# Performance work log

Measured on AMD Instinct MI355X. Metric: run time of the kernel, lower is better.

Reference implementation:

```python
import jax, jax.numpy as jnp
import numpy as np

NUM_FILTER = 256
CAPS_LEN = 8
NUM_EMOTIONS = 8
OUT_DIM = 16
NUM_CHANNEL = 25
TIME_LEN = 25
NUM_CAPS = NUM_CHANNEL * TIME_LEN * (NUM_FILTER // CAPS_LEN)  # 20000
NUM_ITERATIONS = 3


def setup_inputs() -> dict:
    key = jax.random.key(0)
    ks = jax.random.split(key, 10)
    B = 32
    x = jax.random.normal(ks[0], (B, 54, 54), jnp.float32)
    conv1_w = jax.random.normal(ks[1], (NUM_FILTER, 1, 6, 6), jnp.float32) * 0.05
    conv1_b = jax.random.normal(ks[2], (NUM_FILTER,), jnp.float32) * 0.01
    conv2_w = jax.random.normal(ks[3], (NUM_FILTER, NUM_FILTER, 6, 6), jnp.float32) * 0.01
    conv2_b = jax.random.normal(ks[4], (NUM_FILTER,), jnp.float32) * 0.01
    conv3_w = jax.random.normal(ks[5], (NUM_FILTER, 2 * NUM_FILTER, 1, 1), jnp.float32) * 0.05
    conv3_b = jax.random.normal(ks[6], (NUM_FILTER,), jnp.float32) * 0.01
    # PrimaryCaps: one Linear(caps_len -> caps_len) per capsule, batched as [nc, out, in]
    pc_w = jax.random.normal(ks[7], (NUM_CAPS, CAPS_LEN, CAPS_LEN), jnp.float32) * 0.1
    pc_b = jax.random.normal(ks[8], (NUM_CAPS, CAPS_LEN), jnp.float32) * 0.1
    # EmotionCaps transform W: [nc, num_emotions, out_dim, in_dim]
    W = jax.random.normal(ks[9], (NUM_CAPS, NUM_EMOTIONS, OUT_DIM, CAPS_LEN), jnp.float32) * 0.05
    return {"x": x, "conv1_w": conv1_w, "conv1_b": conv1_b, "conv2_w": conv2_w,
            "conv2_b": conv2_b, "conv3_w": conv3_w, "conv3_b": conv3_b,
            "pc_w": pc_w, "pc_b": pc_b, "W": W}


def _conv(x, w, b, stride):
    y = jax.lax.conv_general_dilated(x, w, (stride, stride), 'VALID',
                                     dimension_numbers=('NCHW', 'OIHW', 'NCHW'))
    return y + b[None, :, None, None]


def _squash(s):
    # scale = |s|^2 / (1 + |s|^2); out = scale * s / (|s| + 1e-8)
    n2 = jnp.sum(s * s, axis=-1, keepdims=True)
    n = jnp.sqrt(n2)
    return (n2 / (1.0 + n2)) * s / (n + 1e-8)


def reference(x, conv1_w, conv1_b, conv2_w, conv2_b, conv3_w, conv3_b, pc_w, pc_b, W):
    x4 = x[:, None]                                    # [B,1,54,54]
    x1 = jax.nn.relu(_conv(x4, conv1_w, conv1_b, 2))   # [B,F,25,25]
    y = jnp.pad(x1, ((0, 0), (0, 0), (2, 3), (2, 3)))  # ZeroPad2d((2,3,2,3))
    y = jax.nn.relu(_conv(y, conv2_w, conv2_b, 1))     # [B,F,25,25]
    z = jax.nn.relu(jnp.concatenate([x1, y], axis=1))  # [B,2F,25,25]
    z = _conv(z, conv3_w, conv3_b, 1)                  # [B,F,25,25]
    B, F, H, Wd = z.shape
    # flatten to capsules: [B, F//caps_len, caps_len, H*W] -> [B, nc, caps_len]
    caps = z.reshape(B, F // CAPS_LEN, CAPS_LEN, H * Wd)
    caps = caps.transpose(0, 1, 3, 2).reshape(B, NUM_CAPS, CAPS_LEN)
    # PrimaryCaps: per-capsule linear, batched as a single einsum
    u = jnp.einsum('bni,noi->bno', caps, pc_w) + pc_b[None]   # [B,nc,caps_len]
    # EmotionCaps: u_hat[b,n,e,o] = W[n,e,o,i] u[b,n,i]
    u_hat = jnp.einsum('bni,neoi->bneo', u, W)                # [B,nc,ne,out_dim]
    b = jnp.zeros((B, NUM_CAPS, NUM_EMOTIONS), u.dtype)
    v = None
    for r in range(NUM_ITERATIONS):
        c = jax.nn.softmax(b, axis=2)[..., None]              # [B,nc,ne,1]
        v = _squash(jnp.sum(c * u_hat, axis=1))               # [B,ne,out_dim]
        if r < NUM_ITERATIONS - 1:
            b = b + jnp.einsum('bneo,beo->bne', u_hat, v)
    return jnp.linalg.norm(v, axis=-1)                        # [B,ne]
```

## Files before the change

kernel.cpp:

```cpp
#include <hip/hip_runtime.h>

typedef unsigned short u16;
typedef __attribute__((ext_vector_type(8))) short bf16x8;
typedef __attribute__((ext_vector_type(4))) float floatx4;

#define NPIX 625
#define NCAPS 20000
#define K2 9216

__device__ __forceinline__ u16 f2bf(float f) {
  unsigned u = __float_as_uint(f);
  return (u16)((u + 0x7fffu + ((u >> 16) & 1u)) >> 16);
}

__device__ __forceinline__ float bf2f(unsigned v) {
  return __uint_as_float(v << 16);
}

#define GLDS16(g, l) __builtin_amdgcn_global_load_lds( \
    (const __attribute__((address_space(1))) void*)(g), \
    (__attribute__((address_space(3))) void*)(l), 16, 0, 0)

__global__ void prep_weights2(const float* __restrict__ w2, const float* __restrict__ w3,
                              u16* __restrict__ A2, u16* __restrict__ A3) {
  if (blockIdx.x < 256) {
    const int oc = blockIdx.x, c = threadIdx.x;
    const float* src = w2 + (oc * 256 + c) * 36;
    float v[36];
#pragma unroll
    for (int k = 0; k < 9; k++) {
      const float4 q = *(const float4*)(src + k * 4);
      v[k * 4 + 0] = q.x; v[k * 4 + 1] = q.y; v[k * 4 + 2] = q.z; v[k * 4 + 3] = q.w;
    }
    u16* dst = A2 + oc * 9216 + c;
#pragma unroll
    for (int t = 0; t < 36; t++) dst[t * 256] = f2bf(v[t]);
  } else {
    const int j = (blockIdx.x - 256) * 1024 + threadIdx.x * 4;
    const float4 q = *(const float4*)(w3 + j);
    ushort4 p;
    p.x = f2bf(q.x); p.y = f2bf(q.y); p.z = f2bf(q.z); p.w = f2bf(q.w);
    *(ushort4*)(A3 + j) = p;
  }
}

__global__ void prep_wbs(const float* __restrict__ W, u16* __restrict__ Wbs) {
  int r = blockIdx.x * 256 + threadIdx.x;
  int n = r >> 7, eo = r & 127;
  int e = eo >> 4, o = eo & 15;
  const float* src = W + n * 1024 + eo * 8;
  const float4 v0 = *(const float4*)src;
  const float4 v1 = *(const float4*)(src + 4);
  u16* dst = Wbs + n * 1088 + e * 136 + o * 8;
  ushort4 p0, p1;
  p0.x = f2bf(v0.x); p0.y = f2bf(v0.y); p0.z = f2bf(v0.z); p0.w = f2bf(v0.w);
  p1.x = f2bf(v1.x); p1.y = f2bf(v1.y); p1.z = f2bf(v1.z); p1.w = f2bf(v1.w);
  *(ushort4*)dst = p0;
  *(ushort4*)(dst + 4) = p1;
}

__global__ void conv1_kernel(const float* __restrict__ x, const float* __restrict__ w1,
                             const float* __restrict__ b1, u16* __restrict__ x1p) {
  int blk = blockIdx.x;
  int b = blk / 25, i = blk % 25;
  int f = threadIdx.x;
  float wreg[36];
#pragma unroll
  for (int k = 0; k < 36; k++) wreg[k] = w1[f * 36 + k];
  float bias = b1[f];
  const float* xb = x + b * 54 * 54 + (2 * i) * 54;
  for (int j = 0; j < 25; j++) {
    float acc = bias;
#pragma unroll
    for (int ki = 0; ki < 6; ki++)
#pragma unroll
      for (int kj = 0; kj < 6; kj++)
        acc = fmaf(xb[ki * 54 + 2 * j + kj], wreg[ki * 6 + kj], acc);
    x1p[(((b * 30 + i + 2) * 30) + (j + 2)) * 256 + f] = f2bf(fmaxf(acc, 0.f));
  }
}

__global__ __launch_bounds__(256) void conv2_gemm(const u16* __restrict__ A2,
    const u16* __restrict__ x1p, u16* __restrict__ P) {
  __shared__ u16 As0[128 * 32];
  __shared__ u16 Bs0[128 * 32];
  __shared__ u16 As1[128 * 32];
  __shared__ u16 Bs1[128 * 32];
  const int tid = threadIdx.x;
  const int lane = tid & 63, wave = tid >> 6;
  const int f = blockIdx.x;
  const int xcd = f & 7, ntile = f >> 3;
  const int kt = xcd >> 1, mtile = xcd & 1;
  const int t0 = kt * 9;

  const int seg0 = tid, seg1 = tid + 256;
  const u16* gA0 = A2 + (mtile * 128 + (seg0 >> 2)) * K2 + (seg0 & 3) * 8 + t0 * 256;
  const u16* gA1 = A2 + (mtile * 128 + (seg1 >> 2)) * K2 + (seg1 & 3) * 8 + t0 * 256;

  auto pixbase = [&](int seg) {
    int n = ntile * 128 + (seg >> 2);
    if (n > NCAPS - 1) n = NCAPS - 1;
    int b = n / NPIX, p = n % NPIX;
    int i = p / 25, j = p % 25;
    return ((b * 30 + i) * 30 + j) * 256 + (seg & 3) * 8;
  };
  const u16* gb0 = x1p + pixbase(seg0);
  const u16* gb1 = x1p + pixbase(seg1);

  floatx4 acc[4][4] = {};
  const int wm = wave & 1, wn = wave >> 1;
  const int lrow = lane & 15, kgrp = lane >> 4;

  int kj = t0 % 6;
  int boff = ((t0 / 6) * 30 + kj) * 256;
  for (int t = 0; t < 9; t++) {
#pragma unroll 1
    for (int cc = 0; cc < 8; cc += 2) {
      const int b0 = boff + cc * 32;
      GLDS16(gA0, As0 + seg0 * 8);
      GLDS16(gA1, As0 + seg1 * 8);
      GLDS16(gA0 + 32, As1 + seg0 * 8);
      GLDS16(gA1 + 32, As1 + seg1 * 8);
      GLDS16(gb0 + b0, Bs0 + seg0 * 8);
      GLDS16(gb1 + b0, Bs0 + seg1 * 8);
      GLDS16(gb0 + b0 + 32, Bs1 + seg0 * 8);
      GLDS16(gb1 + b0 + 32, Bs1 + seg1 * 8);
      gA0 += 64; gA1 += 64;
      __syncthreads();
      bf16x8 af[4], bfr[4];
#pragma unroll
      for (int tt = 0; tt < 4; tt++) {
        af[tt]  = *(const bf16x8*)(As0 + (wm * 64 + tt * 16 + lrow) * 32 + kgrp * 8);
        bfr[tt] = *(const bf16x8*)(Bs0 + (wn * 64 + tt * 16 + lrow) * 32 + kgrp * 8);
      }
#pragma unroll
      for (int tm = 0; tm < 4; tm++)
#pragma unroll
        for (int tn = 0; tn < 4; tn++)
          acc[tm][tn] = __builtin_amdgcn_mfma_f32_16x16x32_bf16(af[tm], bfr[tn], acc[tm][tn], 0, 0, 0);
#pragma unroll
      for (int tt = 0; tt < 4; tt++) {
        af[tt]  = *(const bf16x8*)(As1 + (wm * 64 + tt * 16 + lrow) * 32 + kgrp * 8);
        bfr[tt] = *(const bf16x8*)(Bs1 + (wn * 64 + tt * 16 + lrow) * 32 + kgrp * 8);
      }
#pragma unroll
      for (int tm = 0; tm < 4; tm++)
#pragma unroll
        for (int tn = 0; tn < 4; tn++)
          acc[tm][tn] = __builtin_amdgcn_mfma_f32_16x16x32_bf16(af[tm], bfr[tn], acc[tm][tn], 0, 0, 0);
      __syncthreads();
    }
    boff += 256;
    kj++;
    if (kj == 6) { kj = 0; boff += 6144; }
  }

  u16* Pk = P + kt * 5120000;
  const int nb = ntile * 128 + wn * 64;
  const int ocb = mtile * 128 + wm * 64 + kgrp * 4;
#pragma unroll
  for (int tn = 0; tn < 4; tn++) {
    int n = nb + tn * 16 + lrow;
    if (n < NCAPS) {
#pragma unroll
      for (int tm = 0; tm < 4; tm++) {
        int oc = ocb + tm * 16;
        ushort4 pk;
        pk.x = f2bf(acc[tm][tn][0]);
        pk.y = f2bf(acc[tm][tn][1]);
        pk.z = f2bf(acc[tm][tn][2]);
        pk.w = f2bf(acc[tm][tn][3]);
        *(ushort4*)(Pk + n * 256 + oc) = pk;
      }
    }
  }
}

__global__ void conv2_red(const u16* __restrict__ P, const float* __restrict__ bias2,
                          u16* __restrict__ y) {
  const int idx = blockIdx.x * 256 + threadIdx.x;
  const ushort4 p0 = *(const ushort4*)(P + idx * 4);
  const ushort4 p1 = *(const ushort4*)(P + 5120000 + idx * 4);
  const ushort4 p2 = *(const ushort4*)(P + 10240000 + idx * 4);
  const ushort4 p3 = *(const ushort4*)(P + 15360000 + idx * 4);
  const float4 bs = *(const float4*)(bias2 + ((idx * 4) & 255));
  float sx = bf2f(p0.x) + bf2f(p1.x) + bf2f(p2.x) + bf2f(p3.x) + bs.x;
  float sy = bf2f(p0.y) + bf2f(p1.y) + bf2f(p2.y) + bf2f(p3.y) + bs.y;
  float sz = bf2f(p0.z) + bf2f(p1.z) + bf2f(p2.z) + bf2f(p3.z) + bs.z;
  float sw = bf2f(p0.w) + bf2f(p1.w) + bf2f(p2.w) + bf2f(p3.w) + bs.w;
  ushort4 pk;
  pk.x = f2bf(fmaxf(sx, 0.f));
  pk.y = f2bf(fmaxf(sy, 0.f));
  pk.z = f2bf(fmaxf(sz, 0.f));
  pk.w = f2bf(fmaxf(sw, 0.f));
  *(ushort4*)(y + idx * 4) = pk;
}

__global__ __launch_bounds__(256) void conv3_gemm(const u16* __restrict__ A3,
    const u16* __restrict__ x1p, const u16* __restrict__ y,
    const float* __restrict__ bias3, float* __restrict__ z) {
  __shared__ u16 As[128 * 32];
  __shared__ u16 Bs[128 * 32];
  const int tid = threadIdx.x;
  const int lane = tid & 63, wave = tid >> 6;
  const int mtile = blockIdx.x, ntile = blockIdx.y;

  const int seg0 = tid, seg1 = tid + 256;
  const u16* ga0 = A3 + (mtile * 128 + (seg0 >> 2)) * 512 + (seg0 & 3) * 8;
  const u16* ga1 = A3 + (mtile * 128 + (seg1 >> 2)) * 512 + (seg1 & 3) * 8;

  auto mkbases = [&](int seg, const u16*& gx, const u16*& gy) {
    int n = ntile * 128 + (seg >> 2);
    if (n > NCAPS - 1) n = NCAPS - 1;
    int b = n / NPIX, p = n % NPIX;
    int i = p / 25, j = p % 25;
    gx = x1p + ((b * 30 + i + 2) * 30 + (j + 2)) * 256 + (seg & 3) * 8;
    gy = y + n * 256 + (seg & 3) * 8;
  };
  const u16 *gx0, *gy0, *gx1, *gy1;
  mkbases(seg0, gx0, gy0);
  mkbases(seg1, gx1, gy1);

  floatx4 acc[4][4] = {};
  const int wm = wave & 1, wn = wave >> 1;
  const int lrow = lane & 15, kgrp = lane >> 4;

  for (int kc = 0; kc < 16; kc++) {
    const u16* s0 = (kc < 8) ? (gx0 + kc * 32) : (gy0 + (kc - 8) * 32);
    const u16* s1 = (kc < 8) ? (gx1 + kc * 32) : (gy1 + (kc - 8) * 32);
    GLDS16(ga0 + kc * 32, As + seg0 * 8);
    GLDS16(ga1 + kc * 32, As + seg1 * 8);
    GLDS16(s0, Bs + seg0 * 8);
    GLDS16(s1, Bs + seg1 * 8);
    __syncthreads();
    bf16x8 af[4], bfr[4];
#pragma unroll
    for (int tt = 0; tt < 4; tt++) {
      af[tt]  = *(const bf16x8*)(As + (wm * 64 + tt * 16 + lrow) * 32 + kgrp * 8);
      bfr[tt] = *(const bf16x8*)(Bs + (wn * 64 + tt * 16 + lrow) * 32 + kgrp * 8);
    }
#pragma unroll
    for (int tm = 0; tm < 4; tm++)
#pragma unroll
      for (int tn = 0; tn < 4; tn++)
        acc[tm][tn] = __builtin_amdgcn_mfma_f32_16x16x32_bf16(af[tm], bfr[tn], acc[tm][tn], 0, 0, 0);
    __syncthreads();
  }

  const int nb = ntile * 128 + wn * 64;
  const int fb = mtile * 128 + wm * 64 + kgrp * 4;
#pragma unroll
  for (int tn = 0; tn < 4; tn++) {
    int n = nb + tn * 16 + lrow;
    if (n < NCAPS) {
#pragma unroll
      for (int tm = 0; tm < 4; tm++) {
        int f0 = fb + tm * 16;
        float4 v;
        v.x = acc[tm][tn][0] + bias3[f0 + 0];
        v.y = acc[tm][tn][1] + bias3[f0 + 1];
        v.z = acc[tm][tn][2] + bias3[f0 + 2];
        v.w = acc[tm][tn][3] + bias3[f0 + 3];
        *(float4*)(z + n * 256 + f0) = v;
      }
    }
  }
}


__device__ __forceinline__ float dot8v(float4 a0, float4 a1, float4 b0, float4 b1) {
  float s = a0.x * b0.x;
  s = fmaf(a0.y, b0.y, s); s = fmaf(a0.z, b0.z, s); s = fmaf(a0.w, b0.w, s);
  s = fmaf(a1.x, b1.x, s); s = fmaf(a1.y, b1.y, s);
  s = fmaf(a1.z, b1.z, s); s = fmaf(a1.w, b1.w, s);
  return s;
}

__device__ __forceinline__ float dotrow(uint4 w, float4 ua, float4 ub) {
  float s = __uint_as_float(w.x << 16) * ua.x;
  s = fmaf(__uint_as_float(w.x & 0xffff0000u), ua.y, s);
  s = fmaf(__uint_as_float(w.y << 16), ua.z, s);
  s = fmaf(__uint_as_float(w.y & 0xffff0000u), ua.w, s);
  s = fmaf(__uint_as_float(w.z << 16), ub.x, s);
  s = fmaf(__uint_as_float(w.z & 0xffff0000u), ub.y, s);
  s = fmaf(__uint_as_float(w.w << 16), ub.z, s);
  s = fmaf(__uint_as_float(w.w & 0xffff0000u), ub.w, s);
  return s;
}

__global__ void caps_u(const float* __restrict__ z, const float* __restrict__ pcw,
                       const float* __restrict__ pcb, float* __restrict__ u) {
  const int tid = threadIdx.x;
  const int b = tid >> 3, o = tid & 7;
  for (int k = 0; k < 8; k++) {
    const int n = blockIdx.x * 8 + k;
    const int g = n / NPIX, p = n % NPIX;
    const float* zp = z + (b * NPIX + p) * 256 + g * 8;
    float4 c0 = *(const float4*)zp;
    float4 c1 = *(const float4*)(zp + 4);
    const float* pw = pcw + n * 64 + o * 8;
    float4 w0 = *(const float4*)pw;
    float4 w1 = *(const float4*)(pw + 4);
    u[n * 256 + tid] = pcb[n * 8 + o] + dot8v(w0, w1, c0, c1);
  }
}

__global__ void caps_u2(const float* __restrict__ z, const float* __restrict__ pcw,
                        const float* __restrict__ pcb, unsigned* __restrict__ u2) {
  const int tid = threadIdx.x;
  const int b = tid >> 3, o = tid & 7;
  for (int k = 0; k < 8; k++) {
    const int n = blockIdx.x * 8 + k;
    const int g = n / NPIX, p = n % NPIX;
    const float* zp = z + (b * NPIX + p) * 256 + g * 8;
    float4 c0 = *(const float4*)zp;
    float4 c1 = *(const float4*)(zp + 4);
    const float* pw = pcw + n * 64 + o * 8;
    float4 w0 = *(const float4*)pw;
    float4 w1 = *(const float4*)(pw + 4);
    const float myu = pcb[n * 8 + o] + dot8v(w0, w1, c0, c1);
    const float partner = __shfl_xor(myu, 1, 64);
    if (!(o & 1)) {
      unsigned pk = (unsigned)f2bf(myu) | ((unsigned)f2bf(partner) << 16);
      u2[n * 128 + b * 4 + (o >> 1)] = pk;
    }
  }
}

__global__ __launch_bounds__(256, 4) void caps_accb2(const unsigned* __restrict__ u2,
    const u16* __restrict__ Wbs, const float* __restrict__ vsum,
    float* __restrict__ Spart) {
  __shared__ u16 Ws[16 * 1088];
  const int tid = threadIdx.x;
  const int b = tid >> 3, e = tid & 7;
  const int n0 = blockIdx.x * 16;

  const u16* gsrc = Wbs + n0 * 1088;
#pragma unroll
  for (int k = 0; k < 9; k++) {
    const int idx = k * 256 + tid;
    if (idx < 2176) GLDS16(gsrc + idx * 8, Ws + idx * 8);
  }

  const float* vp = vsum + tid * 16;
  const float4 V0 = *(const float4*)vp;
  const float4 V1 = *(const float4*)(vp + 4);
  const float4 V2 = *(const float4*)(vp + 8);
  const float4 V3 = *(const float4*)(vp + 12);
  float s0 = 0.f, s1 = 0.f, s2 = 0.f, s3 = 0.f, s4 = 0.f, s5 = 0.f, s6 = 0.f, s7 = 0.f;
  float s8 = 0.f, s9 = 0.f, s10 = 0.f, s11 = 0.f, s12 = 0.f, s13 = 0.f, s14 = 0.f, s15 = 0.f;

  __syncthreads();

  for (int it = 0; it < 16; it++) {
    const int n = n0 + it;
    const uint4 up = *(const uint4*)(u2 + n * 128 + b * 4);
    float4 ua, ub;
    ua.x = __uint_as_float(up.x << 16); ua.y = __uint_as_float(up.x & 0xffff0000u);
    ua.z = __uint_as_float(up.y << 16); ua.w = __uint_as_float(up.y & 0xffff0000u);
    ub.x = __uint_as_float(up.z << 16); ub.y = __uint_as_float(up.z & 0xffff0000u);
    ub.z = __uint_as_float(up.w << 16); ub.w = __uint_as_float(up.w & 0xffff0000u);

    const u16* Wn = Ws + it * 1088 + e * 136;
    float h0, h1, h2, h3, h4, h5, h6, h7, h8, h9, h10, h11, h12, h13, h14, h15;
#define ROW(o, H) { uint4 w = *(const uint4*)(Wn + (o) * 8); H = dotrow(w, ua, ub); }
    ROW(0, h0)   ROW(1, h1)   ROW(2, h2)   ROW(3, h3)
    ROW(4, h4)   ROW(5, h5)   ROW(6, h6)   ROW(7, h7)
    ROW(8, h8)   ROW(9, h9)   ROW(10, h10) ROW(11, h11)
    ROW(12, h12) ROW(13, h13) ROW(14, h14) ROW(15, h15)
#undef ROW
    float blog = h0 * V0.x;
    blog = fmaf(h1, V0.y, blog);  blog = fmaf(h2, V0.z, blog);  blog = fmaf(h3, V0.w, blog);
    blog = fmaf(h4, V1.x, blog);  blog = fmaf(h5, V1.y, blog);  blog = fmaf(h6, V1.z, blog);
    blog = fmaf(h7, V1.w, blog);  blog = fmaf(h8, V2.x, blog);  blog = fmaf(h9, V2.y, blog);
    blog = fmaf(h10, V2.z, blog); blog = fmaf(h11, V2.w, blog); blog = fmaf(h12, V3.x, blog);
    blog = fmaf(h13, V3.y, blog); blog = fmaf(h14, V3.z, blog); blog = fmaf(h15, V3.w, blog);
    float m = blog;
    m = fmaxf(m, __shfl_xor(m, 1, 64));
    m = fmaxf(m, __shfl_xor(m, 2, 64));
    m = fmaxf(m, __shfl_xor(m, 4, 64));
    float ex = __expf(blog - m);
    float ss = ex;
    ss += __shfl_xor(ss, 1, 64);
    ss += __shfl_xor(ss, 2, 64);
    ss += __shfl_xor(ss, 4, 64);
    const float c = ex / ss;
    s0 = fmaf(c, h0, s0);   s1 = fmaf(c, h1, s1);   s2 = fmaf(c, h2, s2);   s3 = fmaf(c, h3, s3);
    s4 = fmaf(c, h4, s4);   s5 = fmaf(c, h5, s5);   s6 = fmaf(c, h6, s6);   s7 = fmaf(c, h7, s7);
    s8 = fmaf(c, h8, s8);   s9 = fmaf(c, h9, s9);   s10 = fmaf(c, h10, s10); s11 = fmaf(c, h11, s11);
    s12 = fmaf(c, h12, s12); s13 = fmaf(c, h13, s13); s14 = fmaf(c, h14, s14); s15 = fmaf(c, h15, s15);
  }
  float* Sp = Spart + blockIdx.x * 4096 + tid * 16;
  *(float4*)(Sp + 0)  = make_float4(s0, s1, s2, s3);
  *(float4*)(Sp + 4)  = make_float4(s4, s5, s6, s7);
  *(float4*)(Sp + 8)  = make_float4(s8, s9, s10, s11);
  *(float4*)(Sp + 12) = make_float4(s12, s13, s14, s15);
}

__global__ __launch_bounds__(256, 2) void caps_acc(const float* __restrict__ u,
    const float* __restrict__ W, const float* __restrict__ vsum,
    float* __restrict__ Spart) {
  const int tid = threadIdx.x;
  const int b = tid >> 3, e = tid & 7;
  const float* vp = vsum + tid * 16;
  const float4 V0 = *(const float4*)vp;
  const float4 V1 = *(const float4*)(vp + 4);
  const float4 V2 = *(const float4*)(vp + 8);
  const float4 V3 = *(const float4*)(vp + 12);
  float s0 = 0.f, s1 = 0.f, s2 = 0.f, s3 = 0.f, s4 = 0.f, s5 = 0.f, s6 = 0.f, s7 = 0.f;
  float s8 = 0.f, s9 = 0.f, s10 = 0.f, s11 = 0.f, s12 = 0.f, s13 = 0.f, s14 = 0.f, s15 = 0.f;
  const int n0 = blockIdx.x * 16;
  for (int it = 0; it < 16; it++) {
    const int n = n0 + it;
    const float* un = u + n * 256 + (b << 3);
    const float4 u0 = *(const float4*)un;
    const float4 u1 = *(const float4*)(un + 4);
    const float* Wn = W + n * 1024 + e * 128;
    float h0, h1, h2, h3, h4, h5, h6, h7, h8, h9, h10, h11, h12, h13, h14, h15;
#define OST(o, H) { float4 wa = *(const float4*)(Wn + (o) * 8); \
                    float4 wb = *(const float4*)(Wn + (o) * 8 + 4); \
                    H = dot8v(wa, wb, u0, u1); }
    OST(0, h0)  OST(1, h1)  OST(2, h2)  OST(3, h3)
    OST(4, h4)  OST(5, h5)  OST(6, h6)  OST(7, h7)
    OST(8, h8)  OST(9, h9)  OST(10, h10) OST(11, h11)
    OST(12, h12) OST(13, h13) OST(14, h14) OST(15, h15)
#undef OST
    float blog = h0 * V0.x;
    blog = fmaf(h1, V0.y, blog);  blog = fmaf(h2, V0.z, blog);  blog = fmaf(h3, V0.w, blog);
    blog = fmaf(h4, V1.x, blog);  blog = fmaf(h5, V1.y, blog);  blog = fmaf(h6, V1.z, blog);
    blog = fmaf(h7, V1.w, blog);  blog = fmaf(h8, V2.x, blog);  blog = fmaf(h9, V2.y, blog);
    blog = fmaf(h10, V2.z, blog); blog = fmaf(h11, V2.w, blog); blog = fmaf(h12, V3.x, blog);
    blog = fmaf(h13, V3.y, blog); blog = fmaf(h14, V3.z, blog); blog = fmaf(h15, V3.w, blog);
    float m = blog;
    m = fmaxf(m, __shfl_xor(m, 1, 64));
    m = fmaxf(m, __shfl_xor(m, 2, 64));
    m = fmaxf(m, __shfl_xor(m, 4, 64));
    float ex = __expf(blog - m);
    float ss = ex;
    ss += __shfl_xor(ss, 1, 64);
    ss += __shfl_xor(ss, 2, 64);
    ss += __shfl_xor(ss, 4, 64);
    const float c = ex / ss;
    s0 = fmaf(c, h0, s0);   s1 = fmaf(c, h1, s1);   s2 = fmaf(c, h2, s2);   s3 = fmaf(c, h3, s3);
    s4 = fmaf(c, h4, s4);   s5 = fmaf(c, h5, s5);   s6 = fmaf(c, h6, s6);   s7 = fmaf(c, h7, s7);
    s8 = fmaf(c, h8, s8);   s9 = fmaf(c, h9, s9);   s10 = fmaf(c, h10, s10); s11 = fmaf(c, h11, s11);
    s12 = fmaf(c, h12, s12); s13 = fmaf(c, h13, s13); s14 = fmaf(c, h14, s14); s15 = fmaf(c, h15, s15);
  }
  float* Sp = Spart + blockIdx.x * 4096 + tid * 16;
  *(float4*)(Sp + 0)  = make_float4(s0, s1, s2, s3);
  *(float4*)(Sp + 4)  = make_float4(s4, s5, s6, s7);
  *(float4*)(Sp + 8)  = make_float4(s8, s9, s10, s11);
  *(float4*)(Sp + 12) = make_float4(s12, s13, s14, s15);
}

__global__ void caps_redA(const float* __restrict__ Spart, float* __restrict__ S) {
  const int j = blockIdx.x * 256 + threadIdx.x;
  const int r0 = blockIdx.y * 50;
  float a0 = 0.f, a1 = 0.f;
  for (int r = 0; r < 50; r += 2) {
    a0 += Spart[(r0 + r) * 4096 + j];
    a1 += Spart[(r0 + r + 1) * 4096 + j];
  }
  atomicAdd(&S[j], a0 + a1);
}

__global__ void caps_v(const float* __restrict__ S, float* __restrict__ vsum, int add) {
  const int t = threadIdx.x;
  const float* sp = S + t * 16;
  const float4 a0 = *(const float4*)sp;
  const float4 a1 = *(const float4*)(sp + 4);
  const float4 a2 = *(const float4*)(sp + 8);
  const float4 a3 = *(const float4*)(sp + 12);
  float n2 = a0.x * a0.x;
  n2 = fmaf(a0.y, a0.y, n2); n2 = fmaf(a0.z, a0.z, n2); n2 = fmaf(a0.w, a0.w, n2);
  n2 = fmaf(a1.x, a1.x, n2); n2 = fmaf(a1.y, a1.y, n2); n2 = fmaf(a1.z, a1.z, n2); n2 = fmaf(a1.w, a1.w, n2);
  n2 = fmaf(a2.x, a2.x, n2); n2 = fmaf(a2.y, a2.y, n2); n2 = fmaf(a2.z, a2.z, n2); n2 = fmaf(a2.w, a2.w, n2);
  n2 = fmaf(a3.x, a3.x, n2); n2 = fmaf(a3.y, a3.y, n2); n2 = fmaf(a3.z, a3.z, n2); n2 = fmaf(a3.w, a3.w, n2);
  const float n = sqrtf(n2);
  const float scale = n2 / ((1.f + n2) * (n + 1e-8f));
  float* vp = vsum + t * 16;
  float4 o0, o1, o2, o3;
  if (add) {
    o0 = *(float4*)(vp + 0); o1 = *(float4*)(vp + 4); o2 = *(float4*)(vp + 8); o3 = *(float4*)(vp + 12);
  } else {
    o0 = make_float4(0.f, 0.f, 0.f, 0.f); o1 = o0; o2 = o0; o3 = o0;
  }
  o0.x = fmaf(a0.x, scale, o0.x); o0.y = fmaf(a0.y, scale, o0.y);
  o0.z = fmaf(a0.z, scale, o0.z); o0.w = fmaf(a0.w, scale, o0.w);
  o1.x = fmaf(a1.x, scale, o1.x); o1.y = fmaf(a1.y, scale, o1.y);
  o1.z = fmaf(a1.z, scale, o1.z); o1.w = fmaf(a1.w, scale, o1.w);
  o2.x = fmaf(a2.x, scale, o2.x); o2.y = fmaf(a2.y, scale, o2.y);
  o2.z = fmaf(a2.z, scale, o2.z); o2.w = fmaf(a2.w, scale, o2.w);
  o3.x = fmaf(a3.x, scale, o3.x); o3.y = fmaf(a3.y, scale, o3.y);
  o3.z = fmaf(a3.z, scale, o3.z); o3.w = fmaf(a3.w, scale, o3.w);
  *(float4*)(vp + 0) = o0; *(float4*)(vp + 4) = o1;
  *(float4*)(vp + 8) = o2; *(float4*)(vp + 12) = o3;
}

__global__ void caps_out(const float* __restrict__ S, float* __restrict__ out) {
  const int t = threadIdx.x;
  const float* sp = S + t * 16;
  const float4 a0 = *(const float4*)sp;
  const float4 a1 = *(const float4*)(sp + 4);
  const float4 a2 = *(const float4*)(sp + 8);
  const float4 a3 = *(const float4*)(sp + 12);
  float n2 = a0.x * a0.x;
  n2 = fmaf(a0.y, a0.y, n2); n2 = fmaf(a0.z, a0.z, n2); n2 = fmaf(a0.w, a0.w, n2);
  n2 = fmaf(a1.x, a1.x, n2); n2 = fmaf(a1.y, a1.y, n2); n2 = fmaf(a1.z, a1.z, n2); n2 = fmaf(a1.w, a1.w, n2);
  n2 = fmaf(a2.x, a2.x, n2); n2 = fmaf(a2.y, a2.y, n2); n2 = fmaf(a2.z, a2.z, n2); n2 = fmaf(a2.w, a2.w, n2);
  n2 = fmaf(a3.x, a3.x, n2); n2 = fmaf(a3.y, a3.y, n2); n2 = fmaf(a3.z, a3.z, n2); n2 = fmaf(a3.w, a3.w, n2);
  const float n = sqrtf(n2);
  out[t] = n * n2 / ((1.f + n2) * (n + 1e-8f));
}

extern "C" void kernel_launch(void* const* d_in, const int* in_sizes, int n_in,
                              void* d_out, int out_size, void* d_ws, size_t ws_size,
                              hipStream_t stream) {
  const float* x   = (const float*)d_in[0];
  const float* w1  = (const float*)d_in[1];
  const float* b1  = (const float*)d_in[2];
  const float* w2  = (const float*)d_in[3];
  const float* b2  = (const float*)d_in[4];
  const float* w3  = (const float*)d_in[5];
  const float* b3  = (const float*)d_in[6];
  const float* pcw = (const float*)d_in[7];
  const float* pcb = (const float*)d_in[8];
  const float* W   = (const float*)d_in[9];
  float* out = (float*)d_out;

  char* ws = (char*)d_ws;
  const bool use_bf16w = (ws_size >= (size_t)75000000);

  u16*   x1p = (u16*)(ws + 0);
  u16*   A2  = (u16*)(ws + 14745600);
  u16*   A3  = (u16*)(ws + 19464192);
  u16*   y   = (u16*)(ws + 19726336);
  u16*   P   = (u16*)(ws + 29966336);

  u16* Wbs;
  unsigned* u2;
  float *z, *Spart, *u, *S, *vs;
  if (use_bf16w) {
    Wbs   = (u16*)(ws + 0);
    z     = (float*)(ws + 43520000);
    Spart = (float*)(ws + 43520000);
    u2    = (unsigned*)(ws + 64000000);
    S     = (float*)(ws + 74240000);
    vs    = (float*)(ws + 74256384);
    u = nullptr;
  } else {
    Wbs = nullptr; u2 = nullptr;
    z     = (float*)(ws + 29966336);
    Spart = (float*)(ws + 29966336);
    u     = (float*)(ws + 50446336);
    S     = (float*)(ws + 70926336);
    vs    = (float*)(ws + 70942720);
  }

  hipMemsetAsync(x1p, 0, 14745600, stream);
  hipMemsetAsync(vs, 0, 16384, stream);

  prep_weights2<<<384, 256, 0, stream>>>(w2, w3, A2, A3);
  conv1_kernel<<<800, 256, 0, stream>>>(x, w1, b1, x1p);
  conv2_gemm<<<1256, 256, 0, stream>>>(A2, x1p, P);
  conv2_red<<<5000, 256, 0, stream>>>(P, b2, y);
  conv3_gemm<<<dim3(2, 157), 256, 0, stream>>>(A3, x1p, y, b3, z);
  if (use_bf16w) {
    prep_wbs<<<10000, 256, 0, stream>>>(W, Wbs);
    caps_u2<<<2500, 256, 0, stream>>>(z, pcw, pcb, u2);
  } else {
    caps_u<<<2500, 256, 0, stream>>>(z, pcw, pcb, u);
  }

  for (int pass = 0; pass < 3; pass++) {
    if (use_bf16w)
      caps_accb2<<<1250, 256, 0, stream>>>(u2, Wbs, vs, Spart);
    else
      caps_acc<<<1250, 256, 0, stream>>>(u, W, vs, Spart);
    hipMemsetAsync(S, 0, 16384, stream);
    caps_redA<<<dim3(16, 25), 256, 0, stream>>>(Spart, S);
    if (pass == 0)      caps_v<<<1, 256, 0, stream>>>(S, vs, 0);
    else if (pass == 1) caps_v<<<1, 256, 0, stream>>>(S, vs, 1);
    else                caps_out<<<1, 256, 0, stream>>>(S, out);
  }
}
```

Measured before the change: 510.9 us.

## Repack conv2 weights per k-chunk, remap block order, drop atomic reduction memsets

The conv2 weight matrix is repacked so that each (k-chunk, m-tile) combination occupies its own contiguous slab. The block index is remapped so that consecutive blocks on each XCD work on the same weight slab, which is meant to improve L2 reuse of A tiles. In the bf16 path, the capsule routing reduction writes per-row-group partials to a buffer instead of doing atomicAdd into a zeroed S. The single-block v/out kernels then sum the 25 partials, which removes a memset and the atomics each pass but adds a slightly larger final read.

Measured after the change: 503.8 us. No clear change (-1.4%).

```diff
diff --git a/kernel.cpp b/kernel.cpp
--- a/kernel.cpp
+++ b/kernel.cpp
@@ -22,7 +22,7 @@
     (__attribute__((address_space(3))) void*)(l), 16, 0, 0)
 
 __global__ void prep_weights2(const float* __restrict__ w2, const float* __restrict__ w3,
-                              u16* __restrict__ A2, u16* __restrict__ A3) {
+                              u16* __restrict__ A2c, u16* __restrict__ A3) {
   if (blockIdx.x < 256) {
     const int oc = blockIdx.x, c = threadIdx.x;
     const float* src = w2 + (oc * 256 + c) * 36;
@@ -32,9 +32,12 @@
       const float4 q = *(const float4*)(src + k * 4);
       v[k * 4 + 0] = q.x; v[k * 4 + 1] = q.y; v[k * 4 + 2] = q.z; v[k * 4 + 3] = q.w;
     }
-    u16* dst = A2 + oc * 9216 + c;
-#pragma unroll
-    for (int t = 0; t < 36; t++) dst[t * 256] = f2bf(v[t]);
+    const int mtile = oc >> 7, row = oc & 127;
+#pragma unroll
+    for (int t = 0; t < 36; t++) {
+      const int kt = t / 9, tl = t % 9;
+      A2c[(kt * 2 + mtile) * 294912 + row * 2304 + tl * 256 + c] = f2bf(v[t]);
+    }
   } else {
     const int j = (blockIdx.x - 256) * 1024 + threadIdx.x * 4;
     const float4 q = *(const float4*)(w3 + j);
@@ -80,7 +83,7 @@
   }
 }
 
-__global__ __launch_bounds__(256) void conv2_gemm(const u16* __restrict__ A2,
+__global__ __launch_bounds__(256) void conv2_gemm(const u16* __restrict__ A2c,
     const u16* __restrict__ x1p, u16* __restrict__ P) {
   __shared__ u16 As0[128 * 32];
   __shared__ u16 Bs0[128 * 32];
@@ -89,13 +92,14 @@
   const int tid = threadIdx.x;
   const int lane = tid & 63, wave = tid >> 6;
   const int f = blockIdx.x;
-  const int xcd = f & 7, ntile = f >> 3;
-  const int kt = xcd >> 1, mtile = xcd & 1;
+  const int w = (f & 7) * 157 + (f >> 3);
+  const int ntile = w >> 3, combo = w & 7;
+  const int kt = combo >> 1, mtile = combo & 1;
   const int t0 = kt * 9;
 
   const int seg0 = tid, seg1 = tid + 256;
-  const u16* gA0 = A2 + (mtile * 128 + (seg0 >> 2)) * K2 + (seg0 & 3) * 8 + t0 * 256;
-  const u16* gA1 = A2 + (mtile * 128 + (seg1 >> 2)) * K2 + (seg1 & 3) * 8 + t0 * 256;
+  const u16* gA0 = A2c + combo * 294912 + (seg0 >> 2) * 2304 + (seg0 & 3) * 8;
+  const u16* gA1 = A2c + combo * 294912 + (seg1 >> 2) * 2304 + (seg1 & 3) * 8;
 
   auto pixbase = [&](int seg) {
     int n = ntile * 128 + (seg >> 2);
@@ -453,6 +457,80 @@
   *(float4*)(Sp + 12) = make_float4(s12, s13, s14, s15);
 }
 
+__global__ void caps_redB(const float* __restrict__ Spart, float* __restrict__ Sp2) {
+  const int j = blockIdx.x * 256 + threadIdx.x;
+  const int r0 = blockIdx.y * 50;
+  float a0 = 0.f, a1 = 0.f;
+  for (int r = 0; r < 50; r += 2) {
+    a0 += Spart[(r0 + r) * 4096 + j];
+    a1 += Spart[(r0 + r + 1) * 4096 + j];
+  }
+  Sp2[blockIdx.y * 4096 + j] = a0 + a1;
+}
+
+__global__ void caps_v2(const float* __restrict__ Sp2, float* __restrict__ vsum, int add) {
+  const int t = threadIdx.x;
+  float4 a0 = make_float4(0.f, 0.f, 0.f, 0.f), a1 = a0, a2 = a0, a3 = a0;
+  for (int r = 0; r < 25; r++) {
+    const float* sp = Sp2 + r * 4096 + t * 16;
+    const float4 q0 = *(const float4*)sp;
+    const float4 q1 = *(const float4*)(sp + 4);
+    const float4 q2 = *(const float4*)(sp + 8);
+    const float4 q3 = *(const float4*)(sp + 12);
+    a0.x += q0.x; a0.y += q0.y; a0.z += q0.z; a0.w += q0.w;
+    a1.x += q1.x; a1.y += q1.y; a1.z += q1.z; a1.w += q1.w;
+    a2.x += q2.x; a2.y += q2.y; a2.z += q2.z; a2.w += q2.w;
+    a3.x += q3.x; a3.y += q3.y; a3.z += q3.z; a3.w += q3.w;
+  }
+  float n2 = a0.x * a0.x;
+  n2 = fmaf(a0.y, a0.y, n2); n2 = fmaf(a0.z, a0.z, n2); n2 = fmaf(a0.w, a0.w, n2);
+  n2 = fmaf(a1.x, a1.x, n2); n2 = fmaf(a1.y, a1.y, n2); n2 = fmaf(a1.z, a1.z, n2); n2 = fmaf(a1.w, a1.w, n2);
+  n2 = fmaf(a2.x, a2.x, n2); n2 = fmaf(a2.y, a2.y, n2); n2 = fmaf(a2.z, a2.z, n2); n2 = fmaf(a2.w, a2.w, n2);
+  n2 = fmaf(a3.x, a3.x, n2); n2 = fmaf(a3.y, a3.y, n2); n2 = fmaf(a3.z, a3.z, n2); n2 = fmaf(a3.w, a3.w, n2);
+  const float n = sqrtf(n2);
+  const float scale = n2 / ((1.f + n2) * (n + 1e-8f));
+  float* vp = vsum + t * 16;
+  float4 o0, o1, o2, o3;
+  if (add) {
+    o0 = *(float4*)(vp + 0); o1 = *(float4*)(vp + 4); o2 = *(float4*)(vp + 8); o3 = *(float4*)(vp + 12);
+  } else {
+    o0 = make_float4(0.f, 0.f, 0.f, 0.f); o1 = o0; o2 = o0; o3 = o0;
+  }
+  o0.x = fmaf(a0.x, scale, o0.x); o0.y = fmaf(a0.y, scale, o0.y);
+  o0.z = fmaf(a0.z, scale, o0.z); o0.w = fmaf(a0.w, scale, o0.w);
+  o1.x = fmaf(a1.x, scale, o1.x); o1.y = fmaf(a1.y, scale, o1.y);
+  o1.z = fmaf(a1.z, scale, o1.z); o1.w = fmaf(a1.w, scale, o1.w);
+  o2.x = fmaf(a2.x, scale, o2.x); o2.y = fmaf(a2.y, scale, o2.y);
+  o2.z = fmaf(a2.z, scale, o2.z); o2.w = fmaf(a2.w, scale, o2.w);
+  o3.x = fmaf(a3.x, scale, o3.x); o3.y = fmaf(a3.y, scale, o3.y);
+  o3.z = fmaf(a3.z, scale, o3.z); o3.w = fmaf(a3.w, scale, o3.w);
+  *(float4*)(vp + 0) = o0; *(float4*)(vp + 4) = o1;
+  *(float4*)(vp + 8) = o2; *(float4*)(vp + 12) = o3;
+}
+
+__global__ void caps_out2(const float* __restrict__ Sp2, float* __restrict__ out) {
+  const int t = threadIdx.x;
+  float4 a0 = make_float4(0.f, 0.f, 0.f, 0.f), a1 = a0, a2 = a0, a3 = a0;
+  for (int r = 0; r < 25; r++) {
+    const float* sp = Sp2 + r * 4096 + t * 16;
+    const float4 q0 = *(const float4*)sp;
+    const float4 q1 = *(const float4*)(sp + 4);
+    const float4 q2 = *(const float4*)(sp + 8);
+    const float4 q3 = *(const float4*)(sp + 12);
+    a0.x += q0.x; a0.y += q0.y; a0.z += q0.z; a0.w += q0.w;
+    a1.x += q1.x; a1.y += q1.y; a1.z += q1.z; a1.w += q1.w;
+    a2.x += q2.x; a2.y += q2.y; a2.z += q2.z; a2.w += q2.w;
+    a3.x += q3.x; a3.y += q3.y; a3.z += q3.z; a3.w += q3.w;
+  }
+  float n2 = a0.x * a0.x;
+  n2 = fmaf(a0.y, a0.y, n2); n2 = fmaf(a0.z, a0.z, n2); n2 = fmaf(a0.w, a0.w, n2);
+  n2 = fmaf(a1.x, a1.x, n2); n2 = fmaf(a1.y, a1.y, n2); n2 = fmaf(a1.z, a1.z, n2); n2 = fmaf(a1.w, a1.w, n2);
+  n2 = fmaf(a2.x, a2.x, n2); n2 = fmaf(a2.y, a2.y, n2); n2 = fmaf(a2.z, a2.z, n2); n2 = fmaf(a2.w, a2.w, n2);
+  n2 = fmaf(a3.x, a3.x, n2); n2 = fmaf(a3.y, a3.y, n2); n2 = fmaf(a3.z, a3.z, n2); n2 = fmaf(a3.w, a3.w, n2);
+  const float n = sqrtf(n2);
+  out[t] = n * n2 / ((1.f + n2) * (n + 1e-8f));
+}
+
 __global__ void caps_redA(const float* __restrict__ Spart, float* __restrict__ S) {
   const int j = blockIdx.x * 256 + threadIdx.x;
   const int r0 = blockIdx.y * 50;
@@ -539,17 +617,17 @@
 
   u16* Wbs;
   unsigned* u2;
-  float *z, *Spart, *u, *S, *vs;
+  float *z, *Spart, *u, *S, *vs, *Sp2;
   if (use_bf16w) {
     Wbs   = (u16*)(ws + 0);
     z     = (float*)(ws + 43520000);
     Spart = (float*)(ws + 43520000);
     u2    = (unsigned*)(ws + 64000000);
-    S     = (float*)(ws + 74240000);
-    vs    = (float*)(ws + 74256384);
-    u = nullptr;
+    Sp2   = (float*)(ws + 74240000);
+    vs    = (float*)(ws + 74649600);
+    u = nullptr; S = nullptr;
   } else {
-    Wbs = nullptr; u2 = nullptr;
+    Wbs = nullptr; u2 = nullptr; Sp2 = nullptr;
     z     = (float*)(ws + 29966336);
     Spart = (float*)(ws + 29966336);
     u     = (float*)(ws + 50446336);
@@ -573,14 +651,19 @@
   }
 
   for (int pass = 0; pass < 3; pass++) {
-    if (use_bf16w)
+    if (use_bf16w) {
       caps_accb2<<<1250, 256, 0, stream>>>(u2, Wbs, vs, Spart);
-    else
+      caps_redB<<<dim3(16, 25), 256, 0, stream>>>(Spart, Sp2);
+      if (pass == 0)      caps_v2<<<1, 256, 0, stream>>>(Sp2, vs, 0);
+      else if (pass == 1) caps_v2<<<1, 256, 0, stream>>>(Sp2, vs, 1);
+      else                caps_out2<<<1, 256, 0, stream>>>(Sp2, out);
+    } else {
       caps_acc<<<1250, 256, 0, stream>>>(u, W, vs, Spart);
-    hipMemsetAsync(S, 0, 16384, stream);
-    caps_redA<<<dim3(16, 25), 256, 0, stream>>>(Spart, S);
-    if (pass == 0)      caps_v<<<1, 256, 0, stream>>>(S, vs, 0);
-    else if (pass == 1) caps_v<<<1, 256, 0, stream>>>(S, vs, 1);
-    else                caps_out<<<1, 256, 0, stream>>>(S, out);
-  }
-}
+      hipMemsetAsync(S, 0, 16384, stream);
+      caps_redA<<<dim3(16, 25), 256, 0, stream>>>(Spart, S);
+      if (pass == 0)      caps_v<<<1, 256, 0, stream>>>(S, vs, 0);
+      else if (pass == 1) caps_v<<<1, 256, 0, stream>>>(S, vs, 1);
+      else                caps_out<<<1, 256, 0, stream>>>(S, out);
+    }
+  }
+}
```
